# Performance work log

Measured on AMD Instinct MI355X. Metric: run time of the kernel, lower is better.

Reference implementation:

```python
import jax, jax.numpy as jnp
import numpy as np

IN_DIM = 1024
OUT_DIM = 1024
L = 4
HIDDEN = 64
EMB_DIM = 2 + 2 * 2 * L  # 18
BATCH = 8192
W0 = 30.0


def make_embedded_coords():
    gy, gx = jnp.meshgrid(jnp.linspace(-1.0, 1.0, OUT_DIM), jnp.linspace(-1.0, 1.0, IN_DIM), indexing='ij')
    coords = jnp.stack([gy, gx], axis=-1).reshape(-1, 2)  # [rows*cols, 2]
    embeds = [coords]
    for i in range(L):
        freq = 2.0 ** i
        embeds.append(jnp.sin(freq * jnp.pi * coords))
        embeds.append(jnp.cos(freq * jnp.pi * coords))
    return jnp.concatenate(embeds, axis=-1)  # [rows*cols, 18]


def setup_inputs() -> dict:
    key = jax.random.key(0)
    ks = jax.random.split(key, 8)
    # init scales matching torch code
    u = lambda k, shape, b: jax.random.uniform(k, shape, jnp.float32, -b, b)
    W1 = u(ks[0], (HIDDEN, EMB_DIM), 1.0 / EMB_DIM)
    b1 = u(ks[1], (HIDDEN,), 1.0 / np.sqrt(EMB_DIM))
    s2 = np.sqrt(6.0 / HIDDEN) / W0
    W2 = u(ks[2], (HIDDEN, HIDDEN), s2)
    b2 = u(ks[3], (HIDDEN,), 1.0 / np.sqrt(HIDDEN))
    W3 = u(ks[4], (1, HIDDEN), s2)
    b3 = u(ks[5], (1,), 1.0 / np.sqrt(HIDDEN))
    x = jax.random.normal(ks[6], (BATCH, IN_DIM), jnp.float32)
    bias = jnp.zeros((OUT_DIM,), jnp.float32)
    return {
        'x': x,
        'embedded_coords': make_embedded_coords(),
        'W1': W1, 'b1': b1, 'W2': W2, 'b2': b2, 'W3': W3, 'b3': b3,
        'bias': bias,
    }


def reference(x, embedded_coords, W1, b1, W2, b2, W3, b3, bias):
    rows = bias.shape[0]
    cols = x.shape[-1]
    # tiny fully-fused hypernet MLP over rows*cols coordinate points
    h = jnp.sin(W0 * (embedded_coords @ W1.T + b1))  # [rows*cols, 64]
    h = jnp.sin(W0 * (h @ W2.T + b2))                # [rows*cols, 64]
    W = (h @ W3.T + b3).reshape(rows, cols)          # generated weight
    return x @ W.T + bias                            # [batch, out_dim]
```

## Files before the change

kernel.cpp:

```cpp
#include <hip/hip_runtime.h>
#include <hip/hip_bf16.h>


typedef __attribute__((ext_vector_type(8))) short bf16x8;
typedef __attribute__((ext_vector_type(4))) float f32x4;

#define SIN_SCALE 4.77464829275686f

__device__ __forceinline__ unsigned short f2bf(float f) {
    union { float f; unsigned u; } v; v.f = f;
    unsigned r = v.u + 0x7fffu + ((v.u >> 16) & 1u);
    return (unsigned short)(r >> 16);
}

__device__ __forceinline__ unsigned pktrunc(float a, float b) {
    union { float f; unsigned u; } x, y; x.f = a; y.f = b;
    return (x.u >> 16) | (y.u & 0xffff0000u);
}

__device__ __forceinline__ float sinrev(float x) {
    return __builtin_amdgcn_sinf(x);
}

template <int OFF>
__device__ __forceinline__ float swz_add(float v) {
    return v + __int_as_float(__builtin_amdgcn_ds_swizzle(__float_as_int(v), OFF));
}

__device__ __forceinline__ void async_ld16(const void* g, void* l) {
    __builtin_amdgcn_global_load_lds(
        (__attribute__((address_space(1))) void*)g,
        (__attribute__((address_space(3))) void*)l, 16, 0, 0);
}

__global__ __launch_bounds__(256) void tables_kernel(
        const float* __restrict__ ec,
        const float* __restrict__ W1, const float* __restrict__ b1,
        float* __restrict__ Zrow, float* __restrict__ Zcol) {
    int idx = blockIdx.x * 256 + threadIdx.x;
    int j = idx & 63;
    int t = idx >> 6;
    const float* wr = W1 + j * 18;
    if (t < 1024) {
        const float* pe = ec + (long)t * 1024 * 18;
        float z = b1[j];
        #pragma unroll
        for (int i = 0; i < 18; ++i) z += wr[i] * pe[i];
        Zrow[t * 64 + j] = SIN_SCALE * z;
    } else {
        int c = t - 1024;
        const float* pe = ec + (long)c * 18;
        float z = 0.f;
        #pragma unroll
        for (int i = 0; i < 18; ++i) z += wr[i] * (pe[i] - ec[i]);
        Zcol[c * 64 + j] = SIN_SCALE * z;
    }
}

__global__ __launch_bounds__(256, 3) void fused_cast_siren(
        const float4* __restrict__ x, unsigned short* __restrict__ xb,
        const float* __restrict__ Zrow, const float* __restrict__ Zcol,
        const float* __restrict__ W2, const float* __restrict__ b2,
        const float* __restrict__ W3, const float* __restrict__ b3,
        unsigned short* __restrict__ Wout) {
    int bid = blockIdx.x;
    int sb  = bid / 9;
    if (bid - sb * 9 != 0) {
        int cb = bid - sb - 1;
        long i = (long)cb * 256 + threadIdx.x;
        float4 v = x[i];
        ushort4 o;
        o.x = f2bf(v.x); o.y = f2bf(v.y); o.z = f2bf(v.z); o.w = f2bf(v.w);
        *(ushort4*)(xb + i * 4) = o;
        return;
    }

    int lane = threadIdx.x & 63;
    int wv   = threadIdx.x >> 6;
    int ln   = lane & 15;
    int kq   = lane >> 4;

    bf16x8 bfrag[2][4];
    #pragma unroll
    for (int kc = 0; kc < 2; ++kc)
        #pragma unroll
        for (int nt = 0; nt < 4; ++nt) {
            const float* src = W2 + (nt * 16 + ln) * 64 + kc * 32 + kq * 8;
            union { bf16x8 v; unsigned u[4]; } tmp;
            #pragma unroll
            for (int q = 0; q < 4; ++q)
                tmp.u[q] = pktrunc(SIN_SCALE * src[2*q], SIN_SCALE * src[2*q + 1]);
            bfrag[kc][nt] = tmp.v;
        }
    float b2v[4], w3v[4];
    #pragma unroll
    for (int nt = 0; nt < 4; ++nt) {
        b2v[nt] = SIN_SCALE * b2[nt * 16 + ln];
        w3v[nt] = W3[nt * 16 + ln];
    }
    float b3s = b3[0];

    int wid = sb * 4 + wv;
    int r   = wid >> 2;
    int c0  = (wid & 3) * 256;

    const float* zrp = Zrow + (long)r * 64 + kq * 8;
    float zr0[8], zr1[8];
    #pragma unroll
    for (int j = 0; j < 8; ++j) { zr0[j] = zrp[j]; zr1[j] = zrp[32 + j]; }

    for (int it = 0; it < 8; ++it) {
        int ca = c0 + it * 32 + ln;
        const float* zca = Zcol + (long)ca * 64 + kq * 8;
        const float* zcb = zca + 16 * 64;

        float sa0[8], sa1[8], sb0[8], sb1[8];
        #pragma unroll
        for (int j = 0; j < 8; ++j) {
            sa0[j] = sinrev(zr0[j] + zca[j]);
            sa1[j] = sinrev(zr1[j] + zca[32 + j]);
            sb0[j] = sinrev(zr0[j] + zcb[j]);
            sb1[j] = sinrev(zr1[j] + zcb[32 + j]);
        }
        union { bf16x8 v; unsigned u[4]; } a0, a1, bb0, bb1;
        #pragma unroll
        for (int q = 0; q < 4; ++q) {
            a0.u[q]  = pktrunc(sa0[2*q], sa0[2*q + 1]);
            a1.u[q]  = pktrunc(sa1[2*q], sa1[2*q + 1]);
            bb0.u[q] = pktrunc(sb0[2*q], sb0[2*q + 1]);
            bb1.u[q] = pktrunc(sb1[2*q], sb1[2*q + 1]);
        }

        f32x4 acca[4] = {}, accb[4] = {};
        #pragma unroll
        for (int nt = 0; nt < 4; ++nt) {
            acca[nt] = __builtin_amdgcn_mfma_f32_16x16x32_bf16(a0.v,  bfrag[0][nt], acca[nt], 0, 0, 0);
            accb[nt] = __builtin_amdgcn_mfma_f32_16x16x32_bf16(bb0.v, bfrag[0][nt], accb[nt], 0, 0, 0);
            acca[nt] = __builtin_amdgcn_mfma_f32_16x16x32_bf16(a1.v,  bfrag[1][nt], acca[nt], 0, 0, 0);
            accb[nt] = __builtin_amdgcn_mfma_f32_16x16x32_bf16(bb1.v, bfrag[1][nt], accb[nt], 0, 0, 0);
        }

        float pa[4], pb[4];
        #pragma unroll
        for (int rg = 0; rg < 4; ++rg) {
            float s = 0.f, t2 = 0.f;
            #pragma unroll
            for (int nt = 0; nt < 4; ++nt) {
                s  += w3v[nt] * sinrev(acca[nt][rg] + b2v[nt]);
                t2 += w3v[nt] * sinrev(accb[nt][rg] + b2v[nt]);
            }
            pa[rg] = s; pb[rg] = t2;
        }
        #pragma unroll
        for (int rg = 0; rg < 4; ++rg) {
            pa[rg] = swz_add<0x041F>(pa[rg]);  pb[rg] = swz_add<0x041F>(pb[rg]);
            pa[rg] = swz_add<0x081F>(pa[rg]);  pb[rg] = swz_add<0x081F>(pb[rg]);
            pa[rg] = swz_add<0x101F>(pa[rg]);  pb[rg] = swz_add<0x101F>(pb[rg]);
            pa[rg] = swz_add<0x201F>(pa[rg]);  pb[rg] = swz_add<0x201F>(pb[rg]);
        }

        if (ln == 0) {
            long p0 = (long)r * 1024 + c0 + it * 32;
            ushort4 oa, ob;
            oa.x = f2bf(pa[0] + b3s); oa.y = f2bf(pa[1] + b3s);
            oa.z = f2bf(pa[2] + b3s); oa.w = f2bf(pa[3] + b3s);
            ob.x = f2bf(pb[0] + b3s); ob.y = f2bf(pb[1] + b3s);
            ob.z = f2bf(pb[2] + b3s); ob.w = f2bf(pb[3] + b3s);
            *(ushort4*)(Wout + p0 + kq * 4)      = oa;
            *(ushort4*)(Wout + p0 + 16 + kq * 4) = ob;
        }
    }
}

__global__ __launch_bounds__(256) void gemm_kernel(
        const unsigned short* __restrict__ A,
        const unsigned short* __restrict__ B,
        const float* __restrict__ bias,
        float* __restrict__ C) {
    const int K = 1024;
    __shared__ __align__(16) unsigned short As[2][128 * 64];
    __shared__ __align__(16) unsigned short Bs[2][128 * 64];

    int tid  = threadIdx.x;
    int lane = tid & 63;
    int wv   = tid >> 6;
    int wm   = wv & 1, wn = wv >> 1;
    long Abase = (long)blockIdx.x * 128 * K;
    long Bbase = (long)blockIdx.y * 128 * K;

    int sr8 = tid >> 3;
    int sl  = tid & 7;
    int rsel = lane & 15;
    int kq   = lane >> 4;

    f32x4 acc[4][4] = {};

    auto stage = [&](int kt, int sbuf) {
        #pragma unroll
        for (int q = 0; q < 4; ++q) {
            int row = q * 32 + sr8;
            int cc  = sl ^ (row & 7);
            const unsigned short* ga = A + Abase + (long)row * K + kt + cc * 8;
            const unsigned short* gb = B + Bbase + (long)row * K + kt + cc * 8;
            unsigned short* la = &As[sbuf][(q * 256 + wv * 64) * 8];
            unsigned short* lb = &Bs[sbuf][(q * 256 + wv * 64) * 8];
            async_ld16(ga, la);
            async_ld16(gb, lb);
        }
    };

    auto compute = [&](int sbuf) {
        #pragma unroll
        for (int h = 0; h < 2; ++h) {
            bf16x8 af[4], bf[4];
            #pragma unroll
            for (int mi = 0; mi < 4; ++mi) {
                int row = wm * 64 + mi * 16 + rsel;
                int ch  = (h * 4 + kq) ^ (row & 7);
                af[mi] = *(const bf16x8*)&As[sbuf][row * 64 + ch * 8];
            }
            #pragma unroll
            for (int ni = 0; ni < 4; ++ni) {
                int row = wn * 64 + ni * 16 + rsel;
                int ch  = (h * 4 + kq) ^ (row & 7);
                bf[ni] = *(const bf16x8*)&Bs[sbuf][row * 64 + ch * 8];
            }
            #pragma unroll
            for (int mi = 0; mi < 4; ++mi)
                #pragma unroll
                for (int ni = 0; ni < 4; ++ni)
                    acc[mi][ni] = __builtin_amdgcn_mfma_f32_16x16x32_bf16(
                        af[mi], bf[ni], acc[mi][ni], 0, 0, 0);
        }
    };

    stage(0, 0);
    __syncthreads();
    int buf = 0;
    for (int kt = 64; kt < K; kt += 64) {
        stage(kt, buf ^ 1);
        compute(buf);
        __syncthreads();
        buf ^= 1;
    }
    compute(buf);

    int row0 = blockIdx.x * 128 + wm * 64;
    int col0 = blockIdx.y * 128 + wn * 64;
    #pragma unroll
    for (int ni = 0; ni < 4; ++ni) {
        int col = col0 + ni * 16 + rsel;
        float bv = bias[col];
        #pragma unroll
        for (int mi = 0; mi < 4; ++mi) {
            int rbase = row0 + mi * 16 + kq * 4;
            #pragma unroll
            for (int r = 0; r < 4; ++r)
                C[(long)(rbase + r) * 1024 + col] = acc[mi][ni][r] + bv;
        }
    }
}

extern "C" void kernel_launch(void* const* d_in, const int* in_sizes, int n_in,
                              void* d_out, int out_size, void* d_ws, size_t ws_size,
                              hipStream_t stream) {
    const float* x    = (const float*)d_in[0];
    const float* ec   = (const float*)d_in[1];
    const float* W1   = (const float*)d_in[2];
    const float* b1   = (const float*)d_in[3];
    const float* W2   = (const float*)d_in[4];
    const float* b2   = (const float*)d_in[5];
    const float* W3   = (const float*)d_in[6];
    const float* b3   = (const float*)d_in[7];
    const float* bias = (const float*)d_in[8];
    float* out = (float*)d_out;

    unsigned short* xb = (unsigned short*)d_ws;
    unsigned short* Wb = xb + (size_t)8192 * 1024;
    float* Zrow = (float*)(Wb + (size_t)1024 * 1024);
    float* Zcol = Zrow + 1024 * 64;

    tables_kernel<<<512, 256, 0, stream>>>(ec, W1, b1, Zrow, Zcol);
    fused_cast_siren<<<9216, 256, 0, stream>>>((const float4*)x, xb, Zrow, Zcol,
                                               W2, b2, W3, b3, Wb);
    dim3 g(64, 8);
    gemm_kernel<<<g, 256, 0, stream>>>(xb, Wb, bias, out);
}
```

Measured before the change: 215.0 us.

## Use sin angle-addition identity for first SIREN layer and split cast kernel

```diff
diff --git a/kernel.cpp b/kernel.cpp
--- a/kernel.cpp
+++ b/kernel.cpp
@@ -21,6 +21,9 @@
 __device__ __forceinline__ float sinrev(float x) {
     return __builtin_amdgcn_sinf(x);
 }
+__device__ __forceinline__ float cosrev(float x) {
+    return __builtin_amdgcn_cosf(x);
+}
 
 template <int OFF>
 __device__ __forceinline__ float swz_add(float v) {
@@ -36,7 +39,7 @@
 __global__ __launch_bounds__(256) void tables_kernel(
         const float* __restrict__ ec,
         const float* __restrict__ W1, const float* __restrict__ b1,
-        float* __restrict__ Zrow, float* __restrict__ Zcol) {
+        float2* __restrict__ SCrow, float2* __restrict__ SCcol) {
     int idx = blockIdx.x * 256 + threadIdx.x;
     int j = idx & 63;
     int t = idx >> 6;
@@ -46,35 +49,33 @@
         float z = b1[j];
         #pragma unroll
         for (int i = 0; i < 18; ++i) z += wr[i] * pe[i];
-        Zrow[t * 64 + j] = SIN_SCALE * z;
+        z *= SIN_SCALE;
+        SCrow[t * 64 + j] = make_float2(sinrev(z), cosrev(z));
     } else {
         int c = t - 1024;
         const float* pe = ec + (long)c * 18;
         float z = 0.f;
         #pragma unroll
         for (int i = 0; i < 18; ++i) z += wr[i] * (pe[i] - ec[i]);
-        Zcol[c * 64 + j] = SIN_SCALE * z;
-    }
-}
-
-__global__ __launch_bounds__(256, 3) void fused_cast_siren(
-        const float4* __restrict__ x, unsigned short* __restrict__ xb,
-        const float* __restrict__ Zrow, const float* __restrict__ Zcol,
+        z *= SIN_SCALE;
+        SCcol[c * 64 + j] = make_float2(sinrev(z), cosrev(z));
+    }
+}
+
+__global__ __launch_bounds__(256) void cast_kernel(
+        const float4* __restrict__ x, unsigned short* __restrict__ xb) {
+    long i = (long)blockIdx.x * 256 + threadIdx.x;
+    float4 v = x[i];
+    ushort4 o;
+    o.x = f2bf(v.x); o.y = f2bf(v.y); o.z = f2bf(v.z); o.w = f2bf(v.w);
+    *(ushort4*)(xb + i * 4) = o;
+}
+
+__global__ __launch_bounds__(256) void siren_w_kernel(
+        const float2* __restrict__ SCrow, const float2* __restrict__ SCcol,
         const float* __restrict__ W2, const float* __restrict__ b2,
         const float* __restrict__ W3, const float* __restrict__ b3,
         unsigned short* __restrict__ Wout) {
-    int bid = blockIdx.x;
-    int sb  = bid / 9;
-    if (bid - sb * 9 != 0) {
-        int cb = bid - sb - 1;
-        long i = (long)cb * 256 + threadIdx.x;
-        float4 v = x[i];
-        ushort4 o;
-        o.x = f2bf(v.x); o.y = f2bf(v.y); o.z = f2bf(v.z); o.w = f2bf(v.w);
-        *(ushort4*)(xb + i * 4) = o;
-        return;
-    }
-
     int lane = threadIdx.x & 63;
     int wv   = threadIdx.x >> 6;
     int ln   = lane & 15;
@@ -100,27 +101,31 @@
     }
     float b3s = b3[0];
 
-    int wid = sb * 4 + wv;
-    int r   = wid >> 2;
-    int c0  = (wid & 3) * 256;
-
-    const float* zrp = Zrow + (long)r * 64 + kq * 8;
-    float zr0[8], zr1[8];
-    #pragma unroll
-    for (int j = 0; j < 8; ++j) { zr0[j] = zrp[j]; zr1[j] = zrp[32 + j]; }
-
-    for (int it = 0; it < 8; ++it) {
+    int wid = blockIdx.x * 4 + wv;
+    int r   = wid >> 3;
+    int c0  = (wid & 7) * 128;
+
+    const float2* rp = SCrow + (long)r * 64 + kq * 8;
+    float sr0[8], cr0[8], sr1[8], cr1[8];
+    #pragma unroll
+    for (int j = 0; j < 8; ++j) {
+        float2 t0 = rp[j];      sr0[j] = t0.x; cr0[j] = t0.y;
+        float2 t1 = rp[32 + j]; sr1[j] = t1.x; cr1[j] = t1.y;
+    }
+
+    for (int it = 0; it < 4; ++it) {
         int ca = c0 + it * 32 + ln;
-        const float* zca = Zcol + (long)ca * 64 + kq * 8;
-        const float* zcb = zca + 16 * 64;
+        const float2* fa = SCcol + (long)ca * 64 + kq * 8;
+        const float2* fb = fa + 16 * 64;
 
         float sa0[8], sa1[8], sb0[8], sb1[8];
         #pragma unroll
         for (int j = 0; j < 8; ++j) {
-            sa0[j] = sinrev(zr0[j] + zca[j]);
-            sa1[j] = sinrev(zr1[j] + zca[32 + j]);
-            sb0[j] = sinrev(zr0[j] + zcb[j]);
-            sb1[j] = sinrev(zr1[j] + zcb[32 + j]);
+            float2 a0 = fa[j], a1 = fa[32 + j], q0 = fb[j], q1 = fb[32 + j];
+            sa0[j] = fmaf(sr0[j], a0.y, cr0[j] * a0.x);
+            sa1[j] = fmaf(sr1[j], a1.y, cr1[j] * a1.x);
+            sb0[j] = fmaf(sr0[j], q0.y, cr0[j] * q0.x);
+            sb1[j] = fmaf(sr1[j], q1.y, cr1[j] * q1.x);
         }
         union { bf16x8 v; unsigned u[4]; } a0, a1, bb0, bb1;
         #pragma unroll
@@ -277,12 +282,12 @@
 
     unsigned short* xb = (unsigned short*)d_ws;
     unsigned short* Wb = xb + (size_t)8192 * 1024;
-    float* Zrow = (float*)(Wb + (size_t)1024 * 1024);
-    float* Zcol = Zrow + 1024 * 64;
-
-    tables_kernel<<<512, 256, 0, stream>>>(ec, W1, b1, Zrow, Zcol);
-    fused_cast_siren<<<9216, 256, 0, stream>>>((const float4*)x, xb, Zrow, Zcol,
-                                               W2, b2, W3, b3, Wb);
+    float2* SCrow = (float2*)(Wb + (size_t)1024 * 1024);
+    float2* SCcol = SCrow + 1024 * 64;
+
+    tables_kernel<<<512, 256, 0, stream>>>(ec, W1, b1, SCrow, SCcol);
+    cast_kernel<<<8192, 256, 0, stream>>>((const float4*)x, xb);
+    siren_w_kernel<<<2048, 256, 0, stream>>>(SCrow, SCcol, W2, b2, W3, b3, Wb);
     dim3 g(64, 8);
     gemm_kernel<<<g, 256, 0, stream>>>(xb, Wb, bias, out);
 }
```

New measurement: 242.0 us. 1.13x slower.

## Move x cast into table kernel and tile SIREN weight gen through LDS

Applied to the files above, without the earlier changes.

```diff
diff --git a/kernel.cpp b/kernel.cpp
--- a/kernel.cpp
+++ b/kernel.cpp
@@ -33,52 +33,69 @@
         (__attribute__((address_space(3))) void*)l, 16, 0, 0);
 }
 
-__global__ __launch_bounds__(256) void tables_kernel(
+__global__ __launch_bounds__(256) void prep_kernel(
+        const float4* __restrict__ x, unsigned short* __restrict__ xb,
         const float* __restrict__ ec,
         const float* __restrict__ W1, const float* __restrict__ b1,
         float* __restrict__ Zrow, float* __restrict__ Zcol) {
-    int idx = blockIdx.x * 256 + threadIdx.x;
-    int j = idx & 63;
-    int t = idx >> 6;
-    const float* wr = W1 + j * 18;
-    if (t < 1024) {
-        const float* pe = ec + (long)t * 1024 * 18;
-        float z = b1[j];
-        #pragma unroll
-        for (int i = 0; i < 18; ++i) z += wr[i] * pe[i];
-        Zrow[t * 64 + j] = SIN_SCALE * z;
+    int b = blockIdx.x;
+    if (b < 8192) {
+        long i = (long)b * 256 + threadIdx.x;
+        float4 v = x[i];
+        ushort4 o;
+        o.x = f2bf(v.x); o.y = f2bf(v.y); o.z = f2bf(v.z); o.w = f2bf(v.w);
+        *(ushort4*)(xb + i * 4) = o;
     } else {
-        int c = t - 1024;
-        const float* pe = ec + (long)c * 18;
-        float z = 0.f;
-        #pragma unroll
-        for (int i = 0; i < 18; ++i) z += wr[i] * (pe[i] - ec[i]);
-        Zcol[c * 64 + j] = SIN_SCALE * z;
-    }
-}
-
-__global__ __launch_bounds__(256, 3) void fused_cast_siren(
-        const float4* __restrict__ x, unsigned short* __restrict__ xb,
+        int idx = (b - 8192) * 256 + threadIdx.x;
+        int j = idx & 63;
+        int t = idx >> 6;
+        const float* wr = W1 + j * 18;
+        if (t < 1024) {
+            const float* pe = ec + (long)t * 1024 * 18;
+            float z = b1[j];
+            #pragma unroll
+            for (int i = 0; i < 18; ++i) z += wr[i] * pe[i];
+            Zrow[t * 64 + j] = SIN_SCALE * z;
+        } else {
+            int c = t - 1024;
+            const float* pe = ec + (long)c * 18;
+            float z = 0.f;
+            #pragma unroll
+            for (int i = 0; i < 18; ++i) z += wr[i] * (pe[i] - ec[i]);
+            Zcol[c * 64 + j] = SIN_SCALE * z;
+        }
+    }
+}
+
+__global__ __launch_bounds__(256, 4) void siren_w_kernel(
         const float* __restrict__ Zrow, const float* __restrict__ Zcol,
         const float* __restrict__ W2, const float* __restrict__ b2,
         const float* __restrict__ W3, const float* __restrict__ b3,
         unsigned short* __restrict__ Wout) {
-    int bid = blockIdx.x;
-    int sb  = bid / 9;
-    if (bid - sb * 9 != 0) {
-        int cb = bid - sb - 1;
-        long i = (long)cb * 256 + threadIdx.x;
-        float4 v = x[i];
-        ushort4 o;
-        o.x = f2bf(v.x); o.y = f2bf(v.y); o.z = f2bf(v.z); o.w = f2bf(v.w);
-        *(ushort4*)(xb + i * 4) = o;
-        return;
-    }
-
-    int lane = threadIdx.x & 63;
-    int wv   = threadIdx.x >> 6;
+    __shared__ __align__(16) float zrow_l[16 * 64];
+    __shared__ __align__(16) float zcol_l[32 * 64];
+
+    int tid  = threadIdx.x;
+    int lane = tid & 63;
+    int wv   = tid >> 6;
     int ln   = lane & 15;
     int kq   = lane >> 4;
+
+    int br = blockIdx.x & 63;
+    int bc = blockIdx.x >> 6;
+
+    {
+        const float* zr_src = Zrow + (long)br * 16 * 64 + (wv * 64 + lane) * 4;
+        async_ld16(zr_src, zrow_l + wv * 256);
+        #pragma unroll
+        for (int half = 0; half < 2; ++half) {
+            int P  = half * 256 + wv * 64 + lane;
+            int cr = P >> 4;
+            int lc = (P & 15) ^ (cr & 7);
+            const float* src = Zcol + (long)(bc * 32 + cr) * 64 + lc * 4;
+            async_ld16(src, zcol_l + half * 1024 + wv * 256);
+        }
+    }
 
     bf16x8 bfrag[2][4];
     #pragma unroll
@@ -100,74 +117,77 @@
     }
     float b3s = b3[0];
 
-    int wid = sb * 4 + wv;
-    int r   = wid >> 2;
-    int c0  = (wid & 3) * 256;
-
-    const float* zrp = Zrow + (long)r * 64 + kq * 8;
-    float zr0[8], zr1[8];
+    __syncthreads();
+
     #pragma unroll
-    for (int j = 0; j < 8; ++j) { zr0[j] = zrp[j]; zr1[j] = zrp[32 + j]; }
-
-    for (int it = 0; it < 8; ++it) {
-        int ca = c0 + it * 32 + ln;
-        const float* zca = Zcol + (long)ca * 64 + kq * 8;
-        const float* zcb = zca + 16 * 64;
-
-        float sa0[8], sa1[8], sb0[8], sb1[8];
-        #pragma unroll
-        for (int j = 0; j < 8; ++j) {
-            sa0[j] = sinrev(zr0[j] + zca[j]);
-            sa1[j] = sinrev(zr1[j] + zca[32 + j]);
-            sb0[j] = sinrev(zr0[j] + zcb[j]);
-            sb1[j] = sinrev(zr1[j] + zcb[32 + j]);
-        }
-        union { bf16x8 v; unsigned u[4]; } a0, a1, bb0, bb1;
-        #pragma unroll
-        for (int q = 0; q < 4; ++q) {
-            a0.u[q]  = pktrunc(sa0[2*q], sa0[2*q + 1]);
-            a1.u[q]  = pktrunc(sa1[2*q], sa1[2*q + 1]);
-            bb0.u[q] = pktrunc(sb0[2*q], sb0[2*q + 1]);
-            bb1.u[q] = pktrunc(sb1[2*q], sb1[2*q + 1]);
-        }
-
-        f32x4 acca[4] = {}, accb[4] = {};
-        #pragma unroll
-        for (int nt = 0; nt < 4; ++nt) {
-            acca[nt] = __builtin_amdgcn_mfma_f32_16x16x32_bf16(a0.v,  bfrag[0][nt], acca[nt], 0, 0, 0);
-            accb[nt] = __builtin_amdgcn_mfma_f32_16x16x32_bf16(bb0.v, bfrag[0][nt], accb[nt], 0, 0, 0);
-            acca[nt] = __builtin_amdgcn_mfma_f32_16x16x32_bf16(a1.v,  bfrag[1][nt], acca[nt], 0, 0, 0);
-            accb[nt] = __builtin_amdgcn_mfma_f32_16x16x32_bf16(bb1.v, bfrag[1][nt], accb[nt], 0, 0, 0);
-        }
-
-        float pa[4], pb[4];
-        #pragma unroll
-        for (int rg = 0; rg < 4; ++rg) {
-            float s = 0.f, t2 = 0.f;
+    for (int lr4 = 0; lr4 < 4; ++lr4) {
+        int lr = wv * 4 + lr4;
+        const float* zb = zrow_l + lr * 64 + kq * 8;
+        float zr0[8], zr1[8];
+        #pragma unroll
+        for (int j = 0; j < 8; ++j) { zr0[j] = zb[j]; zr1[j] = zb[32 + j]; }
+
+        #pragma unroll
+        for (int ct = 0; ct < 2; ++ct) {
+            int cl = ct * 16 + ln;
+            const float* cb = zcol_l + cl * 64;
+            int sw = cl & 7;
+            float zc0[8], zc1[8];
+            #pragma unroll
+            for (int d = 0; d < 2; ++d) {
+                int p0 = (((2 * kq + d)    ) ^ sw) * 4;
+                int p1 = (((8 + 2 * kq + d)) ^ sw) * 4;
+                #pragma unroll
+                for (int e = 0; e < 4; ++e) {
+                    zc0[d * 4 + e] = cb[p0 + e];
+                    zc1[d * 4 + e] = cb[p1 + e];
+                }
+            }
+
+            float s0[8], s1[8];
+            #pragma unroll
+            for (int j = 0; j < 8; ++j) {
+                s0[j] = sinrev(zr0[j] + zc0[j]);
+                s1[j] = sinrev(zr1[j] + zc1[j]);
+            }
+            union { bf16x8 v; unsigned u[4]; } a0, a1;
+            #pragma unroll
+            for (int q = 0; q < 4; ++q) {
+                a0.u[q] = pktrunc(s0[2*q], s0[2*q + 1]);
+                a1.u[q] = pktrunc(s1[2*q], s1[2*q + 1]);
+            }
+
+            f32x4 acc[4] = {};
             #pragma unroll
             for (int nt = 0; nt < 4; ++nt) {
-                s  += w3v[nt] * sinrev(acca[nt][rg] + b2v[nt]);
-                t2 += w3v[nt] * sinrev(accb[nt][rg] + b2v[nt]);
-            }
-            pa[rg] = s; pb[rg] = t2;
-        }
-        #pragma unroll
-        for (int rg = 0; rg < 4; ++rg) {
-            pa[rg] = swz_add<0x041F>(pa[rg]);  pb[rg] = swz_add<0x041F>(pb[rg]);
-            pa[rg] = swz_add<0x081F>(pa[rg]);  pb[rg] = swz_add<0x081F>(pb[rg]);
-            pa[rg] = swz_add<0x101F>(pa[rg]);  pb[rg] = swz_add<0x101F>(pb[rg]);
-            pa[rg] = swz_add<0x201F>(pa[rg]);  pb[rg] = swz_add<0x201F>(pb[rg]);
-        }
-
-        if (ln == 0) {
-            long p0 = (long)r * 1024 + c0 + it * 32;
-            ushort4 oa, ob;
-            oa.x = f2bf(pa[0] + b3s); oa.y = f2bf(pa[1] + b3s);
-            oa.z = f2bf(pa[2] + b3s); oa.w = f2bf(pa[3] + b3s);
-            ob.x = f2bf(pb[0] + b3s); ob.y = f2bf(pb[1] + b3s);
-            ob.z = f2bf(pb[2] + b3s); ob.w = f2bf(pb[3] + b3s);
-            *(ushort4*)(Wout + p0 + kq * 4)      = oa;
-            *(ushort4*)(Wout + p0 + 16 + kq * 4) = ob;
+                acc[nt] = __builtin_amdgcn_mfma_f32_16x16x32_bf16(a0.v, bfrag[0][nt], acc[nt], 0, 0, 0);
+                acc[nt] = __builtin_amdgcn_mfma_f32_16x16x32_bf16(a1.v, bfrag[1][nt], acc[nt], 0, 0, 0);
+            }
+
+            float pa[4];
+            #pragma unroll
+            for (int rg = 0; rg < 4; ++rg) {
+                float s = 0.f;
+                #pragma unroll
+                for (int nt = 0; nt < 4; ++nt)
+                    s += w3v[nt] * sinrev(acc[nt][rg] + b2v[nt]);
+                pa[rg] = s;
+            }
+            #pragma unroll
+            for (int rg = 0; rg < 4; ++rg) {
+                pa[rg] = swz_add<0x041F>(pa[rg]);
+                pa[rg] = swz_add<0x081F>(pa[rg]);
+                pa[rg] = swz_add<0x101F>(pa[rg]);
+                pa[rg] = swz_add<0x201F>(pa[rg]);
+            }
+
+            if (ln == 0) {
+                long o = (long)(br * 16 + lr) * 1024 + bc * 32 + ct * 16 + kq * 4;
+                ushort4 oa;
+                oa.x = f2bf(pa[0] + b3s); oa.y = f2bf(pa[1] + b3s);
+                oa.z = f2bf(pa[2] + b3s); oa.w = f2bf(pa[3] + b3s);
+                *(ushort4*)(Wout + o) = oa;
+            }
         }
     }
 }
@@ -280,9 +300,8 @@
     float* Zrow = (float*)(Wb + (size_t)1024 * 1024);
     float* Zcol = Zrow + 1024 * 64;
 
-    tables_kernel<<<512, 256, 0, stream>>>(ec, W1, b1, Zrow, Zcol);
-    fused_cast_siren<<<9216, 256, 0, stream>>>((const float4*)x, xb, Zrow, Zcol,
-                                               W2, b2, W3, b3, Wb);
+    prep_kernel<<<8704, 256, 0, stream>>>((const float4*)x, xb, ec, W1, b1, Zrow, Zcol);
+    siren_w_kernel<<<2048, 256, 0, stream>>>(Zrow, Zcol, W2, b2, W3, b3, Wb);
     dim3 g(64, 8);
     gemm_kernel<<<g, 256, 0, stream>>>(xb, Wb, bias, out);
 }
```

After: 197.2 us. -8.3%, faster.
